# Performance work log

Measured on AMD Instinct MI355X. Metric: run time of the kernel, lower is better.

## Reference

```python
import jax, jax.numpy as jnp
import numpy as np

D_MODEL = 256
MAX_ARITY = 32
MAX_DEPTH = 15
VOCAB = 1027
B = 8192
LN_EPS = 1e-5


def setup_inputs() -> dict:
    key = jax.random.key(0)
    ks = jax.random.split(key, 10)
    nid = jax.random.randint(ks[0], (B,), 0, VOCAB)
    child_embs = jax.random.normal(ks[1], (MAX_ARITY, B, D_MODEL), dtype=jnp.float32)
    child_depths = jax.random.randint(ks[2], (MAX_ARITY, B), 0, MAX_DEPTH)
    # learned parameters
    token_emb = jax.random.normal(ks[3], (VOCAB, D_MODEL), dtype=jnp.float32)
    depth_emb = jax.random.normal(ks[4], (MAX_DEPTH, D_MODEL), dtype=jnp.float32)
    idx_emb = jax.random.normal(ks[5], (MAX_ARITY, D_MODEL), dtype=jnp.float32)
    fan_in = D_MODEL * (1 + 3 * MAX_ARITY)  # 24832
    W = jax.random.normal(ks[6], (fan_in, D_MODEL), dtype=jnp.float32) / np.sqrt(fan_in)
    b = jax.random.normal(ks[7], (D_MODEL,), dtype=jnp.float32) * 0.01
    ln_g = jnp.ones((D_MODEL,), dtype=jnp.float32)
    ln_b = jnp.zeros((D_MODEL,), dtype=jnp.float32)
    return {
        "nid": nid,
        "child_embs": child_embs,
        "child_depths": child_depths,
        "token_emb": token_emb,
        "depth_emb": depth_emb,
        "idx_emb": idx_emb,
        "W": W,
        "b": b,
        "ln_g": ln_g,
        "ln_b": ln_b,
    }


def reference(nid, child_embs, child_depths, token_emb, depth_emb, idx_emb, W, b, ln_g, ln_b):
    A, Bsz, D = child_embs.shape  # [32, B, 256]
    e_op = token_emb[nid]  # [B, D]
    ce = jnp.transpose(child_embs, (1, 0, 2))                 # [B, A, D]
    de = jnp.transpose(depth_emb[child_depths], (1, 0, 2))    # [B, A, D]
    ie = jnp.broadcast_to(idx_emb[None, :, :], (Bsz, A, D))   # [B, A, D]
    # interleave per-child (emb_i, depth_i, idx_i) exactly as the python loop concat
    blocks = jnp.stack([ce, de, ie], axis=2).reshape(Bsz, A * 3 * D)  # [B, 3*A*D]
    x = jnp.concatenate([e_op, blocks], axis=-1)  # [B, D*(1+3A)] = [B, 24832]
    h = jax.nn.relu(x @ W + b)  # [B, D]
    mu = jnp.mean(h, axis=-1, keepdims=True)
    var = jnp.mean(jnp.square(h - mu), axis=-1, keepdims=True)
    return (h - mu) * jax.lax.rsqrt(var + LN_EPS) * ln_g + ln_b
```

## Files before the change

kernel.cpp:

```cpp
#include <hip/hip_runtime.h>

#define D_MODEL 256
#define ARITY   32
#define MAXDEP  15
#define VOCABN  1027
#define BATCH   8192
#define KTOT    8192
#define KQ      2048
#define BK      64
#define NSTEP   32
#define LN_EPS  1e-5f

#define WS_CIDXP 0
#define WS_TOP   8192
#define WS_TDEP  271104
#define WS_PART  393984
#define WS_WT    8782592

typedef __attribute__((ext_vector_type(4))) float f32x4;
typedef __attribute__((ext_vector_type(8))) short bf16x8;

__device__ __forceinline__ unsigned int f2bf(float f) {
  unsigned int u = __builtin_bit_cast(unsigned int, f);
  return (u + 0x7fffu + ((u >> 16) & 1u)) >> 16;
}

__global__ __launch_bounds__(256) void build_tables(
    const float* __restrict__ te, const float* __restrict__ de,
    const float* __restrict__ ie, const float* __restrict__ W,
    const float* __restrict__ bvec, float* __restrict__ ws) {
  __shared__ float sh[4352];
  int bid = blockIdx.x, tid = threadIdx.x;

  if (bid < 257) {
    int v0 = bid * 4;
    int cnt = VOCABN - v0; if (cnt > 4) cnt = 4;
    for (int j = 0; j < cnt; ++j) sh[j * 256 + tid] = te[(v0 + j) * 256 + tid];
    for (int j = cnt; j < 4; ++j) sh[j * 256 + tid] = 0.f;
    __syncthreads();
    float a0 = 0.f, a1 = 0.f, a2 = 0.f, a3 = 0.f;
#pragma unroll 8
    for (int k = 0; k < 256; ++k) {
      float wv = W[k * 256 + tid];
      a0 += sh[k] * wv;
      a1 += sh[256 + k] * wv;
      a2 += sh[512 + k] * wv;
      a3 += sh[768 + k] * wv;
    }
    float a4[4] = {a0, a1, a2, a3};
    for (int j = 0; j < cnt; ++j) ws[WS_TOP + (v0 + j) * 256 + tid] = a4[j];

  } else if (bid < 289) {
    int a = bid - 257;
    for (int d = 0; d < MAXDEP; ++d) sh[d * 256 + tid] = de[d * 256 + tid];
    __syncthreads();
    float acc[MAXDEP];
#pragma unroll
    for (int d = 0; d < MAXDEP; ++d) acc[d] = 0.f;
    const float* Wb = W + ((size_t)(512 + 768 * a)) * 256;
#pragma unroll 2
    for (int k = 0; k < 256; ++k) {
      float wv = Wb[(size_t)k * 256 + tid];
#pragma unroll
      for (int d = 0; d < MAXDEP; ++d) acc[d] += sh[d * 256 + k] * wv;
    }
    for (int d = 0; d < MAXDEP; ++d)
      ws[WS_TDEP + (a * MAXDEP + d) * 256 + tid] = acc[d];

  } else if (bid < 321) {
    int a = bid - 289;
    sh[tid] = ie[a * 256 + tid];
    __syncthreads();
    float acc = (a == 0) ? bvec[tid] : 0.f;
    const float* Wb = W + ((size_t)(768 + 768 * a)) * 256;
#pragma unroll 8
    for (int k = 0; k < 256; ++k) acc += sh[k] * Wb[(size_t)k * 256 + tid];
    ws[WS_CIDXP + a * 256 + tid] = acc;

  } else {
    int j = bid - 321;
    int kt = j >> 2, nt = j & 3;
    int kr = tid >> 2, q = tid & 3;
    int kk = kt * 64 + kr;
    int a = kk >> 8, kp = kk & 255;
    const float* src = W + ((size_t)(256 + 768 * a + kp)) * 256 + nt * 64 + q * 16;
    float4 v0 = *(const float4*)(src);
    float4 v1 = *(const float4*)(src + 4);
    float4 v2 = *(const float4*)(src + 8);
    float4 v3 = *(const float4*)(src + 12);
    float* row = sh + kr * 68 + q * 16;
    *(float4*)(row) = v0; *(float4*)(row + 4) = v1;
    *(float4*)(row + 8) = v2; *(float4*)(row + 12) = v3;
    __syncthreads();
    int nl = tid >> 2, c = tid & 3;
#define PK(i) (f2bf(sh[(c * 16 + 2 * (i)) * 68 + nl]) | (f2bf(sh[(c * 16 + 2 * (i) + 1) * 68 + nl]) << 16))
    uint4 u0 = make_uint4(PK(0), PK(1), PK(2), PK(3));
    uint4 u1 = make_uint4(PK(4), PK(5), PK(6), PK(7));
#undef PK
    unsigned short* Wt = (unsigned short*)(ws + WS_WT);
    unsigned short* dst = Wt + (size_t)(nt * 64 + nl) * KTOT + kt * 64 + c * 16;
    *(uint4*)(dst) = u0;
    *(uint4*)(dst + 8) = u1;
  }
}

__global__ __launch_bounds__(512, 4) void gemm_ce(
    const float* __restrict__ ce, float* __restrict__ ws) {
  const unsigned short* Wt = (const unsigned short*)(ws + WS_WT);
  float* part = ws + WS_PART;

  __shared__ uint4 Al[64 * 8];
  __shared__ uint4 Wl[256 * 8];

  int mt = blockIdx.x >> 2, kq = blockIdx.x & 3;
  int m0 = mt * 64;
  int tid = threadIdx.x;
  int lane = tid & 63, wid = tid >> 6;
  int wm = wid & 1, wn = wid >> 1;
  int arow = tid >> 3, acol = tid & 7;
  int wrow = tid >> 3, wcol = tid & 7;

  f32x4 acc[2][4] = {};

  float4 ra0, ra1;
  uint4 rw[4];

#define LOAD_A(KKE) { int kk_ = (KKE); int a_ = kk_ >> 8, kp_ = kk_ & 255;            \
    const float* asrc = ce + ((size_t)a_ * BATCH + m0 + arow) * 256 + kp_ + acol * 8; \
    ra0 = *(const float4*)asrc; ra1 = *(const float4*)(asrc + 4); }
#define LOAD_W(KKE) { int kk_ = (KKE);                                                \
    const unsigned short* wsrc = Wt + kk_ + wcol * 8;                                 \
    _Pragma("unroll")                                                                 \
    for (int i = 0; i < 4; ++i)                                                       \
      rw[i] = *(const uint4*)(wsrc + (size_t)(i * 64 + wrow) * KTOT); }

  LOAD_A(kq * KQ);
  LOAD_W(kq * KQ);

#pragma unroll 1
  for (int t = 0; t < NSTEP; ++t) {
    __syncthreads();
    unsigned int p0 = f2bf(ra0.x) | (f2bf(ra0.y) << 16);
    unsigned int p1 = f2bf(ra0.z) | (f2bf(ra0.w) << 16);
    unsigned int p2 = f2bf(ra1.x) | (f2bf(ra1.y) << 16);
    unsigned int p3 = f2bf(ra1.z) | (f2bf(ra1.w) << 16);
    Al[arow * 8 + (acol ^ (arow & 7))] = make_uint4(p0, p1, p2, p3);
#pragma unroll
    for (int i = 0; i < 4; ++i) {
      int n = i * 64 + wrow;
      Wl[n * 8 + (wcol ^ (n & 7))] = rw[i];
    }
    if (t + 1 < NSTEP) { LOAD_A(kq * KQ + (t + 1) * BK); LOAD_W(kq * KQ + (t + 1) * BK); }
    __syncthreads();
    int r0 = lane & 15, g = lane >> 4;
#pragma unroll
    for (int kg = 0; kg < 2; ++kg) {
      int chunk = kg * 4 + g;
      bf16x8 af[2], bfr[4];
#pragma unroll
      for (int m = 0; m < 2; ++m)
        af[m] = __builtin_bit_cast(bf16x8, Al[(wm * 32 + m * 16 + r0) * 8 + (chunk ^ (r0 & 7))]);
#pragma unroll
      for (int n = 0; n < 4; ++n) {
        int col = wn * 64 + n * 16 + r0;
        bfr[n] = __builtin_bit_cast(bf16x8, Wl[col * 8 + (chunk ^ (r0 & 7))]);
      }
#pragma unroll
      for (int m = 0; m < 2; ++m)
#pragma unroll
        for (int n = 0; n < 4; ++n)
          acc[m][n] = __builtin_amdgcn_mfma_f32_16x16x32_bf16(af[m], bfr[n], acc[m][n], 0, 0, 0);
    }
  }
#undef LOAD_A
#undef LOAD_W

  float* p = part + ((size_t)kq * BATCH + m0) * 256;
  int r0 = lane & 15, g = lane >> 4;
#pragma unroll
  for (int m = 0; m < 2; ++m)
#pragma unroll
    for (int n = 0; n < 4; ++n)
#pragma unroll
      for (int r = 0; r < 4; ++r)
        p[(wm * 32 + m * 16 + g * 4 + r) * 256 + wn * 64 + n * 16 + r0] = acc[m][n][r];
}

__global__ __launch_bounds__(256) void epilogue(
    const int* __restrict__ nid, const int* __restrict__ cdep,
    const float* __restrict__ ws, const float* __restrict__ lng,
    const float* __restrict__ lnb, float* __restrict__ out) {
  __shared__ float h[32][256];
  __shared__ int cdl[32][32];
  __shared__ int nidl[32];
  int m0 = blockIdx.x * 32, tid = threadIdx.x;
#pragma unroll
  for (int i = 0; i < 4; ++i) {
    int idx = i * 256 + tid;
    int a = idx >> 5, r = idx & 31;
    cdl[r][a] = cdep[a * BATCH + m0 + r];
  }
  if (tid < 32) nidl[tid] = nid[m0 + tid];
  __syncthreads();

  int col = tid;
  float ci = 0.f;
#pragma unroll 8
  for (int a = 0; a < ARITY; ++a) ci += ws[WS_CIDXP + a * 256 + col];

  const float* p0 = ws + WS_PART + (size_t)m0 * 256;
  const float* Top = ws + WS_TOP;
  const float* Td  = ws + WS_TDEP;

  for (int r = 0; r < 32; ++r) {
    float v = ci + Top[(size_t)nidl[r] * 256 + col];
#pragma unroll
    for (int q = 0; q < 4; ++q)
      v += p0[(size_t)q * BATCH * 256 + r * 256 + col];
#pragma unroll
    for (int a = 0; a < ARITY; ++a)
      v += Td[(size_t)(a * MAXDEP + cdl[r][a]) * 256 + col];
    h[r][col] = fmaxf(v, 0.f);
  }
  __syncthreads();

  int lane = tid & 63, w = tid >> 6;
  for (int rr = 0; rr < 8; ++rr) {
    int r = w * 8 + rr;
    float x0 = h[r][lane],       x1 = h[r][64 + lane];
    float x2 = h[r][128 + lane], x3 = h[r][192 + lane];
    float s = x0 + x1 + x2 + x3;
    float q = x0 * x0 + x1 * x1 + x2 * x2 + x3 * x3;
#pragma unroll
    for (int off = 32; off >= 1; off >>= 1) {
      s += __shfl_xor(s, off);
      q += __shfl_xor(q, off);
    }
    float mu = s * (1.f / 256.f);
    float var = q * (1.f / 256.f) - mu * mu;
    float rs = rsqrtf(var + LN_EPS);
    float* o = out + (size_t)(m0 + r) * 256;
    o[lane]       = (x0 - mu) * rs * lng[lane]       + lnb[lane];
    o[64 + lane]  = (x1 - mu) * rs * lng[64 + lane]  + lnb[64 + lane];
    o[128 + lane] = (x2 - mu) * rs * lng[128 + lane] + lnb[128 + lane];
    o[192 + lane] = (x3 - mu) * rs * lng[192 + lane] + lnb[192 + lane];
  }
}

extern "C" void kernel_launch(void* const* d_in, const int* in_sizes, int n_in,
                              void* d_out, int out_size, void* d_ws, size_t ws_size,
                              hipStream_t stream) {
  const int*   nid  = (const int*)d_in[0];
  const float* ce   = (const float*)d_in[1];
  const int*   cdep = (const int*)d_in[2];
  const float* te   = (const float*)d_in[3];
  const float* de   = (const float*)d_in[4];
  const float* ie   = (const float*)d_in[5];
  const float* W    = (const float*)d_in[6];
  const float* bv   = (const float*)d_in[7];
  const float* lng  = (const float*)d_in[8];
  const float* lnb  = (const float*)d_in[9];
  float* out = (float*)d_out;
  float* ws  = (float*)d_ws;

  build_tables<<<dim3(833), dim3(256), 0, stream>>>(te, de, ie, W, bv, ws);
  gemm_ce<<<dim3(512), dim3(512), 0, stream>>>(ce, ws);
  epilogue<<<dim3(256), dim3(256), 0, stream>>>(nid, cdep, ws, lng, lnb, out);
}
```

Before: 650.5 us.

## Load GEMM fragments directly from global memory, dropping LDS staging and barriers

The child-embedding GEMM no longer stages A and W tiles through shared memory with two barriers per step. Each wave now loads its MFMA operand fragments straight from global memory into registers, double-buffered across two register sets. Tiles shrink to 32 rows with 4 waves per block, the grid grows to 1024 blocks, and block indices are remapped. This removes LDS traffic and synchronisation, but W fragments are now re-read from global or L2 by every wave and block, and A accesses are less coalesced.

```diff
diff --git a/kernel.cpp b/kernel.cpp
--- a/kernel.cpp
+++ b/kernel.cpp
@@ -7,8 +7,6 @@
 #define BATCH   8192
 #define KTOT    8192
 #define KQ      2048
-#define BK      64
-#define NSTEP   32
 #define LN_EPS  1e-5f
 
 #define WS_CIDXP 0
@@ -104,86 +102,98 @@
   }
 }
 
-__global__ __launch_bounds__(512, 4) void gemm_ce(
-    const float* __restrict__ ce, float* __restrict__ ws) {
+__global__ void gemm_ce(const float* __restrict__ ce, float* __restrict__ ws) {
   const unsigned short* Wt = (const unsigned short*)(ws + WS_WT);
   float* part = ws + WS_PART;
 
-  __shared__ uint4 Al[64 * 8];
-  __shared__ uint4 Wl[256 * 8];
-
-  int mt = blockIdx.x >> 2, kq = blockIdx.x & 3;
-  int m0 = mt * 64;
+  int bid = blockIdx.x;
+  int kq = (bid >> 1) & 3;
+  int mt = (bid >> 3) + ((bid & 1) << 7);
+  int m0 = mt * 32;
   int tid = threadIdx.x;
-  int lane = tid & 63, wid = tid >> 6;
-  int wm = wid & 1, wn = wid >> 1;
-  int arow = tid >> 3, acol = tid & 7;
-  int wrow = tid >> 3, wcol = tid & 7;
+  int lane = tid & 63, wn = tid >> 6;
+  int r15 = lane & 15, g4 = lane >> 4;
+  int klane = g4 * 8;
+
+  const float* pa0 = ce + ((size_t)(kq * 8) * BATCH + m0 + r15) * 256 + klane;
+  const float* pa1 = pa0 + (size_t)16 * 256;
+  const unsigned short* pwb = Wt + (size_t)(wn * 64 + r15) * KTOT + kq * KQ + klane;
+  const unsigned short* pw0 = pwb;
+  const unsigned short* pw1 = pwb + (size_t)16 * KTOT;
+  const unsigned short* pw2 = pwb + (size_t)32 * KTOT;
+  const unsigned short* pw3 = pwb + (size_t)48 * KTOT;
 
   f32x4 acc[2][4] = {};
 
-  float4 ra0, ra1;
-  uint4 rw[4];
-
-#define LOAD_A(KKE) { int kk_ = (KKE); int a_ = kk_ >> 8, kp_ = kk_ & 255;            \
-    const float* asrc = ce + ((size_t)a_ * BATCH + m0 + arow) * 256 + kp_ + acol * 8; \
-    ra0 = *(const float4*)asrc; ra1 = *(const float4*)(asrc + 4); }
-#define LOAD_W(KKE) { int kk_ = (KKE);                                                \
-    const unsigned short* wsrc = Wt + kk_ + wcol * 8;                                 \
-    _Pragma("unroll")                                                                 \
-    for (int i = 0; i < 4; ++i)                                                       \
-      rw[i] = *(const uint4*)(wsrc + (size_t)(i * 64 + wrow) * KTOT); }
-
-  LOAD_A(kq * KQ);
-  LOAD_W(kq * KQ);
-
+  float4 a0loA, a0hiA, a1loA, a1hiA;  uint4 w0A, w1A, w2A, w3A;
+  float4 a0loB, a0hiB, a1loB, a1hiB;  uint4 w0B, w1B, w2B, w3B;
+
+#define ISSUE(S, OFF)                                                   \
+  a0lo##S = *(const float4*)(pa0 + (OFF));                              \
+  a0hi##S = *(const float4*)(pa0 + (OFF) + 4);                          \
+  a1lo##S = *(const float4*)(pa1 + (OFF));                              \
+  a1hi##S = *(const float4*)(pa1 + (OFF) + 4);                          \
+  w0##S = *(const uint4*)(pw0 + (OFF));                                 \
+  w1##S = *(const uint4*)(pw1 + (OFF));                                 \
+  w2##S = *(const uint4*)(pw2 + (OFF));                                 \
+  w3##S = *(const uint4*)(pw3 + (OFF));
+
+#define CVT8(dst, lo, hi) {                                             \
+    unsigned q0 = f2bf(lo.x) | (f2bf(lo.y) << 16);                      \
+    unsigned q1 = f2bf(lo.z) | (f2bf(lo.w) << 16);                      \
+    unsigned q2 = f2bf(hi.x) | (f2bf(hi.y) << 16);                      \
+    unsigned q3 = f2bf(hi.z) | (f2bf(hi.w) << 16);                      \
+    dst = __builtin_bit_cast(bf16x8, make_uint4(q0, q1, q2, q3)); }
+
+#define COMPUTE(S) {                                                    \
+    bf16x8 af0, af1;                                                    \
+    CVT8(af0, a0lo##S, a0hi##S);                                        \
+    CVT8(af1, a1lo##S, a1hi##S);                                        \
+    bf16x8 b0 = __builtin_bit_cast(bf16x8, w0##S);                      \
+    bf16x8 b1 = __builtin_bit_cast(bf16x8, w1##S);                      \
+    bf16x8 b2 = __builtin_bit_cast(bf16x8, w2##S);                      \
+    bf16x8 b3 = __builtin_bit_cast(bf16x8, w3##S);                      \
+    acc[0][0] = __builtin_amdgcn_mfma_f32_16x16x32_bf16(af0, b0, acc[0][0], 0, 0, 0); \
+    acc[0][1] = __builtin_amdgcn_mfma_f32_16x16x32_bf16(af0, b1, acc[0][1], 0, 0, 0); \
+    acc[0][2] = __builtin_amdgcn_mfma_f32_16x16x32_bf16(af0, b2, acc[0][2], 0, 0, 0); \
+    acc[0][3] = __builtin_amdgcn_mfma_f32_16x16x32_bf16(af0, b3, acc[0][3], 0, 0, 0); \
+    acc[1][0] = __builtin_amdgcn_mfma_f32_16x16x32_bf16(af1, b0, acc[1][0], 0, 0, 0); \
+    acc[1][1] = __builtin_amdgcn_mfma_f32_16x16x32_bf16(af1, b1, acc[1][1], 0, 0, 0); \
+    acc[1][2] = __builtin_amdgcn_mfma_f32_16x16x32_bf16(af1, b2, acc[1][2], 0, 0, 0); \
+    acc[1][3] = __builtin_amdgcn_mfma_f32_16x16x32_bf16(af1, b3, acc[1][3], 0, 0, 0); \
+  }
+
+  ISSUE(A, 0);
 #pragma unroll 1
-  for (int t = 0; t < NSTEP; ++t) {
-    __syncthreads();
-    unsigned int p0 = f2bf(ra0.x) | (f2bf(ra0.y) << 16);
-    unsigned int p1 = f2bf(ra0.z) | (f2bf(ra0.w) << 16);
-    unsigned int p2 = f2bf(ra1.x) | (f2bf(ra1.y) << 16);
-    unsigned int p3 = f2bf(ra1.z) | (f2bf(ra1.w) << 16);
-    Al[arow * 8 + (acol ^ (arow & 7))] = make_uint4(p0, p1, p2, p3);
-#pragma unroll
-    for (int i = 0; i < 4; ++i) {
-      int n = i * 64 + wrow;
-      Wl[n * 8 + (wcol ^ (n & 7))] = rw[i];
-    }
-    if (t + 1 < NSTEP) { LOAD_A(kq * KQ + (t + 1) * BK); LOAD_W(kq * KQ + (t + 1) * BK); }
-    __syncthreads();
-    int r0 = lane & 15, g = lane >> 4;
-#pragma unroll
-    for (int kg = 0; kg < 2; ++kg) {
-      int chunk = kg * 4 + g;
-      bf16x8 af[2], bfr[4];
-#pragma unroll
-      for (int m = 0; m < 2; ++m)
-        af[m] = __builtin_bit_cast(bf16x8, Al[(wm * 32 + m * 16 + r0) * 8 + (chunk ^ (r0 & 7))]);
-#pragma unroll
-      for (int n = 0; n < 4; ++n) {
-        int col = wn * 64 + n * 16 + r0;
-        bfr[n] = __builtin_bit_cast(bf16x8, Wl[col * 8 + (chunk ^ (r0 & 7))]);
+  for (int c = 0; c < 8; ++c) {
+#pragma unroll
+    for (int s = 0; s < 8; s += 2) {
+      ISSUE(B, (s + 1) * 32);
+      COMPUTE(A);
+      if (s == 6) {
+        size_t ab = (c == 7) ? 0 : (size_t)BATCH * 256;
+        size_t wb = (c == 7) ? 0 : 256;
+        pa0 += ab; pa1 += ab;
+        pw0 += wb; pw1 += wb; pw2 += wb; pw3 += wb;
+        ISSUE(A, 0);
+      } else {
+        ISSUE(A, (s + 2) * 32);
       }
-#pragma unroll
-      for (int m = 0; m < 2; ++m)
-#pragma unroll
-        for (int n = 0; n < 4; ++n)
-          acc[m][n] = __builtin_amdgcn_mfma_f32_16x16x32_bf16(af[m], bfr[n], acc[m][n], 0, 0, 0);
-    }
-  }
-#undef LOAD_A
-#undef LOAD_W
+      COMPUTE(B);
+    }
+  }
+#undef ISSUE
+#undef CVT8
+#undef COMPUTE
 
   float* p = part + ((size_t)kq * BATCH + m0) * 256;
-  int r0 = lane & 15, g = lane >> 4;
 #pragma unroll
   for (int m = 0; m < 2; ++m)
 #pragma unroll
     for (int n = 0; n < 4; ++n)
 #pragma unroll
       for (int r = 0; r < 4; ++r)
-        p[(wm * 32 + m * 16 + g * 4 + r) * 256 + wn * 64 + n * 16 + r0] = acc[m][n][r];
+        p[(m * 16 + g4 * 4 + r) * 256 + wn * 64 + n * 16 + r15] = acc[m][n][r];
 }
 
 __global__ __launch_bounds__(256) void epilogue(
@@ -264,6 +274,6 @@
   float* ws  = (float*)d_ws;
 
   build_tables<<<dim3(833), dim3(256), 0, stream>>>(te, de, ie, W, bv, ws);
-  gemm_ce<<<dim3(512), dim3(512), 0, stream>>>(ce, ws);
+  gemm_ce<<<dim3(1024), dim3(256), 0, stream>>>(ce, ws);
   epilogue<<<dim3(256), dim3(256), 0, stream>>>(nid, cdep, ws, lng, lnb, out);
 }
```

New measurement: 717.0 us. 10.2% more time.
